# Kernel tuning notes

Measured on AMD Instinct MI355X. Metric: run time of the kernel, lower is better.

Reference implementation:

```python
import jax, jax.numpy as jnp
import numpy as np

EPS = 1e-8

def _cos_loss(a, b):
    # faithful to torch cos_loss: norm = sqrt(sum(x*x)), x / (norm + 1e-8)
    a_norm = jnp.sqrt(jnp.sum(a * a, axis=1, keepdims=True))
    b_norm = jnp.sqrt(jnp.sum(b * b, axis=1, keepdims=True))
    a_n = a / (a_norm + EPS)
    b_n = b / (b_norm + EPS)
    cossim = jnp.sum(a_n * b_n, axis=1)
    return jnp.mean(1.0 - cossim)

def setup_inputs() -> dict:
    key = jax.random.key(0)
    k1, k2, k3 = jax.random.split(key, 3)
    shape = (1, 768, 64, 64)  # [n, c_cat(block2 VGG16 feats), h, w]
    a = jax.random.normal(k1, shape, dtype=jnp.float32)
    b = jax.random.normal(k2, shape, dtype=jnp.float32)
    d = jax.random.normal(k3, shape, dtype=jnp.float32)
    return {"a": a, "b": b, "d": d}

def reference(a, b, d):
    n, c, h, w = a.shape
    hw = h * w
    a_flat = a.reshape(n, c, hw)   # [n, c, hw]
    b_flat = b.reshape(n, c, hw)   # [n, c, h2w2]
    d_flat = d.reshape(n, c, hw)
    # normalize exactly as argmin_cos_distance: sqrt(sum + 1e-8) then /(norm + 1e-8)
    b_norm = jnp.sqrt(jnp.sum(b_flat * b_flat, axis=1, keepdims=True) + EPS)
    b_n = b_flat / (b_norm + EPS)
    a_norm = jnp.sqrt(jnp.sum(a_flat * a_flat, axis=1, keepdims=True) + EPS)
    a_n = a_flat / (a_norm + EPS)
    # cosine distance matrix [n, hw, h2w2]
    d_mat = 1.0 - jnp.einsum('ncp,ncq->npq', a_n, b_n)
    z_best = jnp.argmin(d_mat, axis=2)  # [n, hw]
    # gather matched style features from d
    idx = jnp.broadcast_to(z_best[:, None, :], (n, c, hw))
    target_feats = jnp.take_along_axis(d_flat, idx, axis=2)  # [n, c, hw]
    # NNFM loss between rendered feats and matched style feats (score is detached)
    loss = _cos_loss(a_flat, target_feats)
    z_new = target_feats.reshape(n, c, h, w)
    return (loss, z_new, z_best)
```

## Files before the change

### kernel.cpp

```cpp
#include <hip/hip_runtime.h>
#include <math.h>

#define EPS  1e-8f
#define C    768
#define HW   4096
#define NKB  24
#define NNB  12
#define NBN  32
#define TAU  0.016f
#define NCH_NEW 12
#define NCH_OLD 48
#define NTT  (3 * (HW / 64) * (C / 64))

typedef float  floatx4 __attribute__((ext_vector_type(4)));
typedef short  shortx8 __attribute__((ext_vector_type(8)));
typedef unsigned short ushort_t;
typedef unsigned int   uint_t;
typedef __attribute__((address_space(1))) uint_t as1_uint;
typedef __attribute__((address_space(3))) uint_t as3_uint;

__device__ __forceinline__ ushort_t f2bf(float v) {
    uint_t u = __float_as_uint(v);
    uint_t r = (u + 0x7FFFu + ((u >> 16) & 1u)) >> 16;
    return (ushort_t)r;
}
__device__ __forceinline__ void async_cp16(const ushort_t* g, ushort_t* l) {
    __builtin_amdgcn_global_load_lds((const as1_uint*)g, (as3_uint*)l, 16, 0, 0);
}

__global__ __launch_bounds__(256) void prep_kernel(
    const float* __restrict__ a, const float* __restrict__ b,
    ushort_t* __restrict__ Ah, ushort_t* __restrict__ Bh,
    float* __restrict__ nbp2, float* __restrict__ out)
{
    __shared__ float tile[64][65];
    const int t = threadIdx.x;
    const int p0 = blockIdx.x * 64;
    const int c0 = blockIdx.y * 64;
    const int r16 = t >> 4;
    const int q4  = (t & 15) * 4;
    const int pl = t >> 2, g = t & 3;
    const int pg = p0 + pl;
    const int sw = (pg >> 1) & 3;

    if (blockIdx.x == 0 && blockIdx.y == 0 && t == 0) out[0] = 0.f;

#pragma unroll
    for (int pp = 0; pp < 4; ++pp) {
        int c = pp * 16 + r16;
        float4 v = *(const float4*)&b[(size_t)(c0 + c) * HW + p0 + q4];
        tile[c][q4]     = v.x; tile[c][q4 + 1] = v.y;
        tile[c][q4 + 2] = v.z; tile[c][q4 + 3] = v.w;
    }
    __syncthreads();
#pragma unroll
    for (int h = 0; h < 2; ++h) {
        const int kb = (c0 >> 5) + h;
        uint_t w[4];
#pragma unroll
        for (int u = 0; u < 4; ++u) {
            ushort_t lo = f2bf(tile[h * 32 + g * 8 + 2 * u][pl]);
            ushort_t hi = f2bf(tile[h * 32 + g * 8 + 2 * u + 1][pl]);
            w[u] = (uint_t)lo | ((uint_t)hi << 16);
        }
        uint4* oh = (uint4*)(Bh + ((size_t)kb * HW + pg) * 32);
        oh[g ^ sw] = make_uint4(w[0], w[1], w[2], w[3]);
    }
    if (t < 64) {
        float s = 0.f;
#pragma unroll
        for (int c = 0; c < 64; ++c) { float v = tile[c][t]; s += v * v; }
        nbp2[blockIdx.y * HW + p0 + t] = s;
    }
    __syncthreads();

#pragma unroll
    for (int pp = 0; pp < 4; ++pp) {
        int c = pp * 16 + r16;
        float4 v = *(const float4*)&a[(size_t)(c0 + c) * HW + p0 + q4];
        tile[c][q4]     = v.x; tile[c][q4 + 1] = v.y;
        tile[c][q4 + 2] = v.z; tile[c][q4 + 3] = v.w;
    }
    __syncthreads();
#pragma unroll
    for (int h = 0; h < 2; ++h) {
        const int kb = (c0 >> 5) + h;
        uint_t w[4];
#pragma unroll
        for (int u = 0; u < 4; ++u) {
            ushort_t lo = f2bf(tile[h * 32 + g * 8 + 2 * u][pl]);
            ushort_t hi = f2bf(tile[h * 32 + g * 8 + 2 * u + 1][pl]);
            w[u] = (uint_t)lo | ((uint_t)hi << 16);
        }
        uint4* oh = (uint4*)(Ah + ((size_t)kb * HW + pg) * 32);
        oh[g ^ sw] = make_uint4(w[0], w[1], w[2], w[3]);
    }
}

__global__ __launch_bounds__(256, 4) void gemm_mfma_kernel(
    const ushort_t* __restrict__ Ah, const ushort_t* __restrict__ Bh,
    const float* __restrict__ nbp2,
    const float* __restrict__ a, const float* __restrict__ b,
    const float* __restrict__ d,
    float* __restrict__ dT, float* __restrict__ bT,
    float* __restrict__ aT, int at_ok,
    float* __restrict__ pv1, int* __restrict__ pi1,
    float* __restrict__ pv2, int* __restrict__ pi2)
{
    __shared__ __align__(16) char smem[33280];
    ushort_t* sA0 = (ushort_t*)smem;
    ushort_t* sB0 = (ushort_t*)(smem + 8192);
    ushort_t* sA1 = (ushort_t*)(smem + 16384);
    ushort_t* sB1 = (ushort_t*)(smem + 24576);
    float*    nb_s = (float*)(smem + 32768);

    const int tid  = threadIdx.x;
    const int lane = tid & 63;
    const int wave = tid >> 6;
    const int wm = wave >> 1, wn = wave & 1;
    const int flat = blockIdx.y * (HW / 128) + blockIdx.x;
    const int orig = (flat & 7) * 128 + (flat >> 3);
    const int bm = orig >> 5, bn = orig & 31;
    const int l15 = lane & 15, l4 = lane >> 4;
    const int swz = (l15 >> 1) & 3;

    floatx4 acc[4][4];
#pragma unroll
    for (int i = 0; i < 4; ++i)
#pragma unroll
        for (int j = 0; j < 4; ++j) acc[i][j] = (floatx4){0.f, 0.f, 0.f, 0.f};

    auto stage = [&](int kb, ushort_t* dA, ushort_t* dB) {
        const size_t aoff = (size_t)(kb * HW + bm * 128) * 32 + tid * 8;
        const size_t boff = (size_t)(kb * HW + bn * 128) * 32 + tid * 8;
        async_cp16(Ah + aoff,        dA + tid * 8);
        async_cp16(Ah + aoff + 2048, dA + tid * 8 + 2048);
        async_cp16(Bh + boff,        dB + tid * 8);
        async_cp16(Bh + boff + 2048, dB + tid * 8 + 2048);
    };
    auto compute = [&](const ushort_t* pA, const ushort_t* pB) {
        shortx8 af[4], bf_[4];
#pragma unroll
        for (int i = 0; i < 4; ++i)
            af[i] = *(const shortx8*)&pA[((wm * 4 + i) * 16 + l15) * 32 + ((l4 ^ swz) * 8)];
#pragma unroll
        for (int j = 0; j < 4; ++j)
            bf_[j] = *(const shortx8*)&pB[((wn * 4 + j) * 16 + l15) * 32 + ((l4 ^ swz) * 8)];
#pragma unroll
        for (int i = 0; i < 4; ++i)
#pragma unroll
            for (int j = 0; j < 4; ++j)
                acc[i][j] = __builtin_amdgcn_mfma_f32_16x16x32_bf16(af[i], bf_[j], acc[i][j], 0, 0, 0);
    };

    stage(0, sA0, sB0);
    if (tid < 128) {
        float s = 0.f;
        int q = bn * 128 + tid;
#pragma unroll
        for (int ch = 0; ch < NNB; ++ch) s += nbp2[ch * HW + q];
        nb_s[tid] = 1.0f / (sqrtf(s + EPS) + EPS);
    }
    __syncthreads();

    for (int kb = 0; kb < NKB; kb += 2) {
        stage(kb + 1, sA1, sB1);
        compute(sA0, sB0);
        __syncthreads();
        if (kb + 2 < NKB) stage(kb + 2, sA0, sB0);
        compute(sA1, sB1);
        __syncthreads();
    }

    float rnb[4];
#pragma unroll
    for (int j = 0; j < 4; ++j)
        rnb[j] = nb_s[wn * 64 + j * 16 + l15];

    float* lv1 = (float*)smem;
    int*   li1 = (int*)(smem + 1024);
    float* lv2 = (float*)(smem + 2048);
    int*   li2 = (int*)(smem + 3072);

#pragma unroll
    for (int i = 0; i < 4; ++i) {
#pragma unroll
        for (int r = 0; r < 4; ++r) {
            float v1 = -INFINITY, v2 = -INFINITY; int i1 = 0, i2 = 0;
#pragma unroll
            for (int j = 0; j < 4; ++j) {
                float sv = acc[i][j][r] * rnb[j];
                int q = bn * 128 + wn * 64 + j * 16 + l15;
                if (sv > v1) { v2 = v1; i2 = i1; v1 = sv; i1 = q; }
                else if (sv > v2) { v2 = sv; i2 = q; }
            }
#pragma unroll
            for (int m = 1; m < 16; m <<= 1) {
                float ov1 = __shfl_xor(v1, m, 64);
                int   oi1 = __shfl_xor(i1, m, 64);
                float ov2 = __shfl_xor(v2, m, 64);
                int   oi2 = __shfl_xor(i2, m, 64);
                if (ov1 > v1 || (ov1 == v1 && oi1 < i1)) {
                    if (v1 > ov2 || (v1 == ov2 && i1 < oi2)) { v2 = v1; i2 = i1; }
                    else { v2 = ov2; i2 = oi2; }
                    v1 = ov1; i1 = oi1;
                } else if (ov1 > v2 || (ov1 == v2 && oi1 < i2)) {
                    v2 = ov1; i2 = oi1;
                }
            }
            if (l15 == 0) {
                int pl = wm * 64 + i * 16 + l4 * 4 + r;
                lv1[pl * 2 + wn] = v1; li1[pl * 2 + wn] = i1;
                lv2[pl * 2 + wn] = v2; li2[pl * 2 + wn] = i2;
            }
        }
    }
    __syncthreads();
    if (tid < 128) {
        float v1 = lv1[tid * 2],     v2 = lv2[tid * 2];
        int   i1 = li1[tid * 2],     i2 = li2[tid * 2];
        float w1 = lv1[tid * 2 + 1], w2 = lv2[tid * 2 + 1];
        int   j1 = li1[tid * 2 + 1], j2 = li2[tid * 2 + 1];
        if (w1 > v1 || (w1 == v1 && j1 < i1)) {
            if (v1 > w2 || (v1 == w2 && i1 < j2)) { v2 = v1; i2 = i1; }
            else { v2 = w2; i2 = j2; }
            v1 = w1; i1 = j1;
        } else if (w1 > v2 || (w1 == v2 && j1 < i2)) {
            v2 = w1; i2 = j1;
        }
        int p = bm * 128 + tid;
        pv1[p * NBN + bn] = v1; pi1[p * NBN + bn] = i1;
        pv2[p * NBN + bn] = v2; pi2[p * NBN + bn] = i2;
    }

    __syncthreads();
    {
        float (*tile)[65] = (float (*)[65])smem;
        const int r16 = tid >> 4;
        const int q4  = (tid & 15) * 4;
        const int flatb = blockIdx.y * (HW / 128) + blockIdx.x;
        for (int tt = flatb; tt < NTT; tt += 1024) {
            const int which = tt / 768;
            const int idx = tt - which * 768;
            if (which == 2 && !at_ok) break;
            const float* src = (which == 0) ? d : ((which == 1) ? b : a);
            float*       dst = (which == 0) ? dT : ((which == 1) ? bT : aT);
            const int tp0 = (idx & 63) * 64;
            const int tc0 = (idx >> 6) * 64;
#pragma unroll
            for (int pp = 0; pp < 4; ++pp) {
                int c = pp * 16 + r16;
                float4 v = *(const float4*)&src[(size_t)(tc0 + c) * HW + tp0 + q4];
                tile[c][q4]     = v.x; tile[c][q4 + 1] = v.y;
                tile[c][q4 + 2] = v.z; tile[c][q4 + 3] = v.w;
            }
            __syncthreads();
#pragma unroll
            for (int pp = 0; pp < 4; ++pp) {
                int p = pp * 16 + r16;
                float4 v;
                v.x = tile[q4][p];     v.y = tile[q4 + 1][p];
                v.z = tile[q4 + 2][p]; v.w = tile[q4 + 3][p];
                *(float4*)&dst[(size_t)(tp0 + p) * C + tc0 + q4] = v;
            }
            __syncthreads();
        }
    }
}

__global__ __launch_bounds__(256) void reduce_recheck_kernel(
    const float* __restrict__ a, const float* __restrict__ b,
    const float* __restrict__ bT, int bt_ok,
    const float* __restrict__ aT, int at_ok,
    const float* __restrict__ pv1, const int* __restrict__ pi1,
    const float* __restrict__ pv2, const int* __restrict__ pi2,
    int* __restrict__ zb, float* __restrict__ out_zbest)
{
    const int wave = threadIdx.x >> 6, lane = threadIdx.x & 63;
    const int p = blockIdx.x * 4 + wave;
    const int tq = lane & 31;

    float v1, v2, candv; int i1, cand;
    if (lane < 32) {
        v1 = pv1[p * NBN + tq]; i1 = pi1[p * NBN + tq]; v2 = pv2[p * NBN + tq];
        cand = i1; candv = v1;
    } else {
        v1 = -INFINITY; v2 = -INFINITY; i1 = 0x7fffffff;
        cand = pi2[p * NBN + tq];
        candv = pv2[p * NBN + tq];
    }
#pragma unroll
    for (int m = 1; m < 32; m <<= 1) {
        float ov1 = __shfl_xor(v1, m, 64);
        int   oi1 = __shfl_xor(i1, m, 64);
        float ov2 = __shfl_xor(v2, m, 64);
        if (ov1 > v1 || (ov1 == v1 && oi1 < i1)) {
            v2 = fmaxf(v1, ov2); v1 = ov1; i1 = oi1;
        } else {
            v2 = fmaxf(v2, ov1);
        }
    }
    v1 = __shfl(v1, 0, 64); v2 = __shfl(v2, 0, 64); i1 = __shfl(i1, 0, 64);

    if (v1 - v2 >= TAU) {
        if (lane == 0) { zb[p] = i1; out_zbest[p] = (float)i1; }
        return;
    }

    const bool active = candv >= v1 - TAU;

    int q = cand;
    float dot = 0.f, b2 = 0.f;
    if (active) {
        if (at_ok) {
            const float* br = bT + (size_t)q * C;
            const float* ar = aT + (size_t)p * C;
#pragma unroll 4
            for (int c = 0; c < C; c += 4) {
                float4 bv = *(const float4*)(br + c);
                float4 av = *(const float4*)(ar + c);
                dot += av.x * bv.x + av.y * bv.y + av.z * bv.z + av.w * bv.w;
                b2  += bv.x * bv.x + bv.y * bv.y + bv.z * bv.z + bv.w * bv.w;
            }
        } else if (bt_ok) {
            const float* br = bT + (size_t)q * C;
            const float* ap = a + p;
#pragma unroll 4
            for (int c = 0; c < C; c += 4) {
                float4 bv = *(const float4*)(br + c);
                dot += ap[(size_t)c * HW] * bv.x + ap[(size_t)(c + 1) * HW] * bv.y
                     + ap[(size_t)(c + 2) * HW] * bv.z + ap[(size_t)(c + 3) * HW] * bv.w;
                b2  += bv.x * bv.x + bv.y * bv.y + bv.z * bv.z + bv.w * bv.w;
            }
        } else {
#pragma unroll 8
            for (int c = 0; c < C; ++c) {
                float av = a[c * HW + p];
                float bv = b[c * HW + q];
                dot += av * bv; b2 += bv * bv;
            }
        }
    }
    float s = active ? (dot / (sqrtf(b2 + EPS) + EPS)) : -INFINITY;
#pragma unroll
    for (int m = 1; m < 64; m <<= 1) {
        float os = __shfl_xor(s, m, 64);
        int   oq = __shfl_xor(q, m, 64);
        if (os > s || (os == s && oq < q)) { s = os; q = oq; }
    }
    if (lane == 0) { zb[p] = q; out_zbest[p] = (float)q; }
}

__global__ __launch_bounds__(256) void gather_loss_kernel(
    const float* __restrict__ a, const float* __restrict__ dT,
    const int* __restrict__ zb, float* __restrict__ out,
    float* __restrict__ pdot, float* __restrict__ pa2, float* __restrict__ pt2)
{
    __shared__ float tile[64][65];
    __shared__ int qs[64];
    const int t = threadIdx.x;
    const int p0 = blockIdx.x * 64;
    const int c0 = blockIdx.y * 64;
    if (t < 64) qs[t] = zb[p0 + t];
    __syncthreads();

    {
        const int pl = t >> 2, sub = t & 3;
        const float* src = dT + (size_t)qs[pl] * C + c0 + sub * 16;
        float4 v0 = *(const float4*)(src);
        float4 v1 = *(const float4*)(src + 4);
        float4 v2 = *(const float4*)(src + 8);
        float4 v3 = *(const float4*)(src + 12);
        float* dst = &tile[pl][sub * 16];
        dst[0] = v0.x; dst[1] = v0.y; dst[2]  = v0.z; dst[3]  = v0.w;
        dst[4] = v1.x; dst[5] = v1.y; dst[6]  = v1.z; dst[7]  = v1.w;
        dst[8] = v2.x; dst[9] = v2.y; dst[10] = v2.z; dst[11] = v2.w;
        dst[12] = v3.x; dst[13] = v3.y; dst[14] = v3.z; dst[15] = v3.w;
    }
    __syncthreads();

    const int p = t & 63, cg = t >> 6;
    float dot = 0.f, a2 = 0.f, t2 = 0.f;
#pragma unroll
    for (int i = 0; i < 16; ++i) {
        int cc = cg * 16 + i;
        float tv = tile[p][cc];
        float av = a[(size_t)(c0 + cc) * HW + p0 + p];
        out[1 + (size_t)(c0 + cc) * HW + p0 + p] = tv;
        dot += av * tv; a2 += av * av; t2 += tv * tv;
    }
    __shared__ float r1[256], r2[256], r3[256];
    r1[t] = dot; r2[t] = a2; r3[t] = t2;
    __syncthreads();
    if (t < 64) {
        dot = r1[t] + r1[t + 64] + r1[t + 128] + r1[t + 192];
        a2  = r2[t] + r2[t + 64] + r2[t + 128] + r2[t + 192];
        t2  = r3[t] + r3[t + 64] + r3[t + 128] + r3[t + 192];
        pdot[blockIdx.y * HW + p0 + t] = dot;
        pa2[blockIdx.y * HW + p0 + t]  = a2;
        pt2[blockIdx.y * HW + p0 + t]  = t2;
    }
}

__global__ __launch_bounds__(256) void loss_finalize_kernel(
    const float* __restrict__ pdot, const float* __restrict__ pa2,
    const float* __restrict__ pt2, float* __restrict__ out, int nch)
{
    int p4 = (blockIdx.x * 256 + threadIdx.x) * 4;
    float d0 = 0.f, d1 = 0.f, d2 = 0.f, d3 = 0.f;
    float a0 = 0.f, a1 = 0.f, a2 = 0.f, a3 = 0.f;
    float t0 = 0.f, t1 = 0.f, t2 = 0.f, t3 = 0.f;
    for (int ch = 0; ch < nch; ++ch) {
        float4 dv = *(const float4*)&pdot[(size_t)ch * HW + p4];
        float4 av = *(const float4*)&pa2[(size_t)ch * HW + p4];
        float4 tv = *(const float4*)&pt2[(size_t)ch * HW + p4];
        d0 += dv.x; d1 += dv.y; d2 += dv.z; d3 += dv.w;
        a0 += av.x; a1 += av.y; a2 += av.z; a3 += av.w;
        t0 += tv.x; t1 += tv.y; t2 += tv.z; t3 += tv.w;
    }
    float contrib =
        (1.f - d0 / ((sqrtf(a0) + EPS) * (sqrtf(t0) + EPS))) +
        (1.f - d1 / ((sqrtf(a1) + EPS) * (sqrtf(t1) + EPS))) +
        (1.f - d2 / ((sqrtf(a2) + EPS) * (sqrtf(t2) + EPS))) +
        (1.f - d3 / ((sqrtf(a3) + EPS) * (sqrtf(t3) + EPS)));
    __shared__ float red[256];
    red[threadIdx.x] = contrib;
    __syncthreads();
    for (int s = 128; s > 0; s >>= 1) {
        if (threadIdx.x < s) red[threadIdx.x] += red[threadIdx.x + s];
        __syncthreads();
    }
    if (threadIdx.x == 0) atomicAdd(out, red[0] * (1.0f / HW));
}

__global__ __launch_bounds__(256) void bnorm_partial_fb_kernel(
    const float* __restrict__ b, float* __restrict__ nbp)
{
    int q = blockIdx.x * 256 + threadIdx.x;
    int c0 = blockIdx.y * 32;
    float s = 0.f;
#pragma unroll 8
    for (int c = c0; c < c0 + 32; ++c) { float v = b[c * HW + q]; s += v * v; }
    nbp[blockIdx.y * HW + q] = s;
}

__global__ __launch_bounds__(256) void bnorm_finalize_fb_kernel(
    const float* __restrict__ nbp, float* __restrict__ nb)
{
    int q = blockIdx.x * 256 + threadIdx.x;
    float s = 0.f;
#pragma unroll
    for (int ch = 0; ch < NKB; ++ch) s += nbp[ch * HW + q];
    nb[q] = sqrtf(s + EPS) + EPS;
}

__global__ __launch_bounds__(256) void gemm_argmax_fb_kernel(
    const float* __restrict__ A, const float* __restrict__ B,
    const float* __restrict__ nb,
    float* __restrict__ pval, int* __restrict__ pidx)
{
    __shared__ __align__(16) char smem[16384];
    float (*As)[128] = (float (*)[128])smem;
    float (*Bs)[128] = (float (*)[128])(smem + 4096);
    const int m0 = blockIdx.x * 128, q0 = blockIdx.y * 128;
    const int tid = threadIdx.x;
    const int tx = tid & 15, ty = tid >> 4;
    const int lr = tid >> 5, lc = (tid & 31) * 4;
    float acc[8][8] = {};
    for (int k0 = 0; k0 < C; k0 += 8) {
        *(float4*)&As[lr][lc] = *(const float4*)&A[(k0 + lr) * HW + m0 + lc];
        *(float4*)&Bs[lr][lc] = *(const float4*)&B[(k0 + lr) * HW + q0 + lc];
        __syncthreads();
#pragma unroll
        for (int kk = 0; kk < 8; ++kk) {
            float a8[8], b8[8];
            *(float4*)&a8[0] = *(float4*)&As[kk][ty * 8];
            *(float4*)&a8[4] = *(float4*)&As[kk][ty * 8 + 4];
            *(float4*)&b8[0] = *(float4*)&Bs[kk][tx * 8];
            *(float4*)&b8[4] = *(float4*)&Bs[kk][tx * 8 + 4];
#pragma unroll
            for (int i = 0; i < 8; ++i)
#pragma unroll
                for (int j = 0; j < 8; ++j) acc[i][j] += a8[i] * b8[j];
        }
        __syncthreads();
    }
    float nbv[8];
#pragma unroll
    for (int j = 0; j < 8; ++j) nbv[j] = nb[q0 + tx * 8 + j];
    float (*rv)[16] = (float (*)[16])smem;
    int   (*ri)[16] = (int   (*)[16])(smem + 8192);
#pragma unroll
    for (int i = 0; i < 8; ++i) {
        float bv = -INFINITY; int bi = 0;
#pragma unroll
        for (int j = 0; j < 8; ++j) {
            float s = acc[i][j] / nbv[j];
            int q = q0 + tx * 8 + j;
            if (s > bv) { bv = s; bi = q; }
        }
        rv[ty * 8 + i][tx] = bv;
        ri[ty * 8 + i][tx] = bi;
    }
    __syncthreads();
    if (tid < 128) {
        float bv = rv[tid][0]; int bi = ri[tid][0];
#pragma unroll
        for (int t = 1; t < 16; ++t) {
            float v = rv[tid][t]; int ii = ri[tid][t];
            if (v > bv || (v == bv && ii < bi)) { bv = v; bi = ii; }
        }
        pval[(m0 + tid) * NBN + blockIdx.y] = bv;
        pidx[(m0 + tid) * NBN + blockIdx.y] = bi;
    }
}

__global__ __launch_bounds__(256) void reduce_fb_kernel(
    const float* __restrict__ pval, const int* __restrict__ pidx,
    int* __restrict__ zb, float* __restrict__ out_zbest)
{
    int p = blockIdx.x * 256 + threadIdx.x;
    float bv = pval[p * NBN]; int bi = pidx[p * NBN];
#pragma unroll 8
    for (int t = 1; t < NBN; ++t) {
        float v = pval[p * NBN + t]; int ii = pidx[p * NBN + t];
        if (v > bv || (v == bv && ii < bi)) { bv = v; bi = ii; }
    }
    zb[p] = bi;
    out_zbest[p] = (float)bi;
}

__global__ __launch_bounds__(256) void gather_partial_kernel(
    const float* __restrict__ a, const float* __restrict__ d,
    const int* __restrict__ zb, float* __restrict__ out,
    float* __restrict__ pdot, float* __restrict__ pa2, float* __restrict__ pt2)
{
    int p = blockIdx.x * 256 + threadIdx.x;
    int ch = blockIdx.y;
    int c0 = ch * (C / NCH_OLD);
    int q = zb[p];
    float dot = 0.f, a2 = 0.f, t2 = 0.f;
#pragma unroll
    for (int c = c0; c < c0 + C / NCH_OLD; ++c) {
        float av = a[c * HW + p];
        float tv = d[c * HW + q];
        dot += av * tv; a2 += av * av; t2 += tv * tv;
        out[1 + c * HW + p] = tv;
    }
    pdot[ch * HW + p] = dot;
    pa2[ch * HW + p] = a2;
    pt2[ch * HW + p] = t2;
}

extern "C" void kernel_launch(void* const* d_in, const int* in_sizes, int n_in,
                              void* d_out, int out_size, void* d_ws, size_t ws_size,
                              hipStream_t stream) {
    const float* a = (const float*)d_in[0];
    const float* b = (const float*)d_in[1];
    const float* d = (const float*)d_in[2];
    float* out = (float*)d_out;
    float* out_zbest = out + 1 + (size_t)C * HW;

    char* ws = (char*)d_ws;
    size_t off = 0;
    auto alloc = [&](size_t bytes) { void* p = ws + off; off = (off + bytes + 255) & ~(size_t)255; return p; };

    const size_t PACK = (size_t)C * HW * 2;
    ushort_t* Ah = (ushort_t*)alloc(PACK);
    ushort_t* Bh = (ushort_t*)alloc(PACK);
    float* nbp = (float*)alloc((size_t)NKB * HW * 4);
    float* pv1 = (float*)alloc((size_t)HW * NBN * 4);
    int*   pi1 = (int*)alloc((size_t)HW * NBN * 4);
    float* pv2 = (float*)alloc((size_t)HW * NBN * 4);
    int*   pi2 = (int*)alloc((size_t)HW * NBN * 4);
    int*   zb  = (int*)alloc(HW * 4);
    float* pdot = (float*)alloc((size_t)NCH_NEW * HW * 4);
    float* pa2  = (float*)alloc((size_t)NCH_NEW * HW * 4);
    float* pt2  = (float*)alloc((size_t)NCH_NEW * HW * 4);
    float* dT  = (float*)alloc((size_t)C * HW * 4);
    float* bT  = (float*)alloc((size_t)C * HW * 4);
    bool fast = off <= ws_size;
    float* aT  = (float*)alloc((size_t)C * HW * 4);
    int at_ok = (off <= ws_size) ? 1 : 0;

    if (fast) {
        prep_kernel<<<dim3(HW / 64, C / 64), 256, 0, stream>>>(
            a, b, Ah, Bh, nbp, out);
        gemm_mfma_kernel<<<dim3(HW / 128, HW / 128), 256, 0, stream>>>(
            Ah, Bh, nbp, a, b, d, dT, bT, aT, at_ok, pv1, pi1, pv2, pi2);
        reduce_recheck_kernel<<<HW / 4, 256, 0, stream>>>(
            a, b, bT, 1, aT, at_ok, pv1, pi1, pv2, pi2, zb, out_zbest);
        gather_loss_kernel<<<dim3(HW / 64, NCH_NEW), 256, 0, stream>>>(
            a, dT, zb, out, pdot, pa2, pt2);
        loss_finalize_kernel<<<HW / 1024, 256, 0, stream>>>(pdot, pa2, pt2, out, NCH_NEW);
    } else {
        off = 0;
        float* nb = (float*)alloc(HW * 4);
        nbp = (float*)alloc((size_t)NKB * HW * 4);
        pv1 = (float*)alloc((size_t)HW * NBN * 4);
        pi1 = (int*)alloc((size_t)HW * NBN * 4);
        zb  = (int*)alloc(HW * 4);
        float* pdot2 = (float*)alloc((size_t)NCH_OLD * HW * 4);
        float* pa22  = (float*)alloc((size_t)NCH_OLD * HW * 4);
        float* pt22  = (float*)alloc((size_t)NCH_OLD * HW * 4);
        hipMemsetAsync(d_out, 0, sizeof(float), stream);
        bnorm_partial_fb_kernel<<<dim3(HW / 256, NKB), 256, 0, stream>>>(b, nbp);
        bnorm_finalize_fb_kernel<<<HW / 256, 256, 0, stream>>>(nbp, nb);
        gemm_argmax_fb_kernel<<<dim3(HW / 128, HW / 128), 256, 0, stream>>>(a, b, nb, pv1, pi1);
        reduce_fb_kernel<<<HW / 256, 256, 0, stream>>>(pv1, pi1, zb, out_zbest);
        gather_partial_kernel<<<dim3(HW / 256, NCH_OLD), 256, 0, stream>>>(
            a, d, zb, out, pdot2, pa22, pt22);
        loss_finalize_kernel<<<HW / 1024, 256, 0, stream>>>(pdot2, pa22, pt22, out, NCH_OLD);
    }
}
```

Baseline: 168.0 us.

## Cooperative wave-wide recheck dot products and fuse loss finalize via last-block counter

The recheck path now has the whole wavefront compute each candidate's dot product together. Each lane covers 12 channels and the partial sums are combined with xor-shuffles, replacing the old scheme where each lane walked a full 768-length row on its own. This gives coalesced loads and spreads the work of a few active candidates across all lanes. The loss finalize kernel is also removed: the last gather block per column (found with an atomic counter that prep_kernel zeroes) sums the channel partials and atomically adds to the loss. This saves one launch, at the cost of nondeterministic float atomic ordering and extra fences.

After: 223.3 us. +32.9%, slower.

```diff
diff --git a/kernel.cpp b/kernel.cpp
--- a/kernel.cpp
+++ b/kernel.cpp
@@ -31,7 +31,8 @@
 __global__ __launch_bounds__(256) void prep_kernel(
     const float* __restrict__ a, const float* __restrict__ b,
     ushort_t* __restrict__ Ah, ushort_t* __restrict__ Bh,
-    float* __restrict__ nbp2, float* __restrict__ out)
+    float* __restrict__ nbp2, int* __restrict__ cntx,
+    float* __restrict__ out)
 {
     __shared__ float tile[64][65];
     const int t = threadIdx.x;
@@ -43,7 +44,10 @@
     const int pg = p0 + pl;
     const int sw = (pg >> 1) & 3;
 
-    if (blockIdx.x == 0 && blockIdx.y == 0 && t == 0) out[0] = 0.f;
+    if (blockIdx.x == 0 && blockIdx.y == 0) {
+        if (t == 0) out[0] = 0.f;
+        if (t < 64) cntx[t] = 0;
+    }
 
 #pragma unroll
     for (int pp = 0; pp < 4; ++pp) {
@@ -309,20 +313,43 @@
 
     const bool active = candv >= v1 - TAU;
 
+    if (at_ok) {
+        unsigned long long mset = __ballot(active);
+        const float* ar = aT + (size_t)p * C + lane * 12;
+        float4 a0 = *(const float4*)ar;
+        float4 a1 = *(const float4*)(ar + 4);
+        float4 a2v = *(const float4*)(ar + 8);
+        float bests = -INFINITY; int bestq = 0x7fffffff;
+        while (mset) {
+            const int src = __ffsll(mset) - 1;
+            mset &= mset - 1;
+            const int qc = __shfl(cand, src, 64);
+            const float* br = bT + (size_t)qc * C + lane * 12;
+            float4 b0 = *(const float4*)br;
+            float4 b1 = *(const float4*)(br + 4);
+            float4 b2v = *(const float4*)(br + 8);
+            float dot = a0.x * b0.x + a0.y * b0.y + a0.z * b0.z + a0.w * b0.w
+                      + a1.x * b1.x + a1.y * b1.y + a1.z * b1.z + a1.w * b1.w
+                      + a2v.x * b2v.x + a2v.y * b2v.y + a2v.z * b2v.z + a2v.w * b2v.w;
+            float bb  = b0.x * b0.x + b0.y * b0.y + b0.z * b0.z + b0.w * b0.w
+                      + b1.x * b1.x + b1.y * b1.y + b1.z * b1.z + b1.w * b1.w
+                      + b2v.x * b2v.x + b2v.y * b2v.y + b2v.z * b2v.z + b2v.w * b2v.w;
+#pragma unroll
+            for (int m = 1; m < 64; m <<= 1) {
+                dot += __shfl_xor(dot, m, 64);
+                bb  += __shfl_xor(bb, m, 64);
+            }
+            const float s = dot / (sqrtf(bb + EPS) + EPS);
+            if (s > bests || (s == bests && qc < bestq)) { bests = s; bestq = qc; }
+        }
+        if (lane == 0) { zb[p] = bestq; out_zbest[p] = (float)bestq; }
+        return;
+    }
+
     int q = cand;
     float dot = 0.f, b2 = 0.f;
     if (active) {
-        if (at_ok) {
-            const float* br = bT + (size_t)q * C;
-            const float* ar = aT + (size_t)p * C;
-#pragma unroll 4
-            for (int c = 0; c < C; c += 4) {
-                float4 bv = *(const float4*)(br + c);
-                float4 av = *(const float4*)(ar + c);
-                dot += av.x * bv.x + av.y * bv.y + av.z * bv.z + av.w * bv.w;
-                b2  += bv.x * bv.x + bv.y * bv.y + bv.z * bv.z + bv.w * bv.w;
-            }
-        } else if (bt_ok) {
+        if (bt_ok) {
             const float* br = bT + (size_t)q * C;
             const float* ap = a + p;
 #pragma unroll 4
@@ -354,10 +381,12 @@
 __global__ __launch_bounds__(256) void gather_loss_kernel(
     const float* __restrict__ a, const float* __restrict__ dT,
     const int* __restrict__ zb, float* __restrict__ out,
-    float* __restrict__ pdot, float* __restrict__ pa2, float* __restrict__ pt2)
+    float* __restrict__ pdot, float* __restrict__ pa2, float* __restrict__ pt2,
+    int* __restrict__ cntx)
 {
     __shared__ float tile[64][65];
     __shared__ int qs[64];
+    __shared__ int lastflag;
     const int t = threadIdx.x;
     const int p0 = blockIdx.x * 64;
     const int c0 = blockIdx.y * 64;
@@ -400,6 +429,30 @@
         pa2[blockIdx.y * HW + p0 + t]  = a2;
         pt2[blockIdx.y * HW + p0 + t]  = t2;
     }
+
+    __threadfence();
+    __syncthreads();
+    if (t == 0)
+        lastflag = (atomicAdd(&cntx[blockIdx.x], 1) == NCH_NEW - 1) ? 1 : 0;
+    __syncthreads();
+    if (lastflag) {
+        __threadfence();
+        if (t < 64) {
+            const int pp = p0 + t;
+            float fd = 0.f, fa = 0.f, ft = 0.f;
+#pragma unroll
+            for (int ch = 0; ch < NCH_NEW; ++ch) {
+                fd += pdot[(size_t)ch * HW + pp];
+                fa += pa2[(size_t)ch * HW + pp];
+                ft += pt2[(size_t)ch * HW + pp];
+            }
+            float contrib = 1.f - fd / ((sqrtf(fa) + EPS) * (sqrtf(ft) + EPS));
+#pragma unroll
+            for (int m = 1; m < 64; m <<= 1)
+                contrib += __shfl_xor(contrib, m, 64);
+            if (t == 0) atomicAdd(out, contrib * (1.0f / HW));
+        }
+    }
 }
 
 __global__ __launch_bounds__(256) void loss_finalize_kernel(
@@ -577,6 +630,7 @@
     float* pdot = (float*)alloc((size_t)NCH_NEW * HW * 4);
     float* pa2  = (float*)alloc((size_t)NCH_NEW * HW * 4);
     float* pt2  = (float*)alloc((size_t)NCH_NEW * HW * 4);
+    int*   cntx = (int*)alloc(64 * 4);
     float* dT  = (float*)alloc((size_t)C * HW * 4);
     float* bT  = (float*)alloc((size_t)C * HW * 4);
     bool fast = off <= ws_size;
@@ -585,14 +639,13 @@
 
     if (fast) {
         prep_kernel<<<dim3(HW / 64, C / 64), 256, 0, stream>>>(
-            a, b, Ah, Bh, nbp, out);
+            a, b, Ah, Bh, nbp, cntx, out);
         gemm_mfma_kernel<<<dim3(HW / 128, HW / 128), 256, 0, stream>>>(
             Ah, Bh, nbp, a, b, d, dT, bT, aT, at_ok, pv1, pi1, pv2, pi2);
         reduce_recheck_kernel<<<HW / 4, 256, 0, stream>>>(
             a, b, bT, 1, aT, at_ok, pv1, pi1, pv2, pi2, zb, out_zbest);
         gather_loss_kernel<<<dim3(HW / 64, NCH_NEW), 256, 0, stream>>>(
-            a, dT, zb, out, pdot, pa2, pt2);
-        loss_finalize_kernel<<<HW / 1024, 256, 0, stream>>>(pdot, pa2, pt2, out, NCH_NEW);
+            a, dT, zb, out, pdot, pa2, pt2, cntx);
     } else {
         off = 0;
         float* nb = (float*)alloc(HW * 4);
```
